# Kernel optimization log

Measured on AMD Instinct MI355X. Metric: run time of the kernel, lower is better.

The kernel has to match this reference:

```python
import jax, jax.numpy as jnp
import numpy as np

N_NODES = 50000
N_EDGES = 800000
N_GRAPHS = 64
NEG_SLOPE = 0.2  # PyG GATConv default negative_slope


def gat_conv(x, src, dst, W, att_src, att_dst, bias, heads, out_ch, concat):
    """PyG-style GATConv (eval mode, self-loops already in src/dst)."""
    N = x.shape[0]
    h = (x @ W).reshape(N, heads, out_ch)            # [N,H,C]
    a_s = jnp.sum(h * att_src, axis=-1)              # [N,H]
    a_d = jnp.sum(h * att_dst, axis=-1)              # [N,H]
    e = jax.nn.leaky_relu(a_s[src] + a_d[dst], NEG_SLOPE)  # [E,H]
    # segment softmax over incoming edges of each dst node
    m = jax.ops.segment_max(e, dst, num_segments=N)
    m = jnp.where(jnp.isfinite(m), m, 0.0)
    ex = jnp.exp(e - m[dst])
    denom = jax.ops.segment_sum(ex, dst, num_segments=N)
    alpha = ex / (denom[dst] + 1e-16)                # [E,H]
    out = jax.ops.segment_sum(alpha[:, :, None] * h[src], dst, num_segments=N)  # [N,H,C]
    out = out.reshape(N, heads * out_ch) if concat else out.mean(axis=1)
    return out + bias


def setup_inputs() -> dict:
    key = jax.random.key(0)
    ks = jax.random.split(key, 12)
    x = jax.random.normal(ks[0], (N_NODES, 5), dtype=jnp.float32)
    edge_index = jax.random.randint(ks[1], (2, N_EDGES), 0, N_NODES, dtype=jnp.int64)
    batch = jnp.sort(jax.random.randint(ks[2], (N_NODES,), 0, N_GRAPHS, dtype=jnp.int64))
    def glorot(k, shape):
        fan_in, fan_out = shape[0], shape[-1]
        s = jnp.sqrt(6.0 / (fan_in + fan_out))
        return jax.random.uniform(k, shape, jnp.float32, -s, s)
    return {
        "x": x,
        "edge_index": edge_index,
        "batch": batch,
        "W1": glorot(ks[3], (5, 256)),
        "att_src1": glorot(ks[4], (4, 64)),
        "att_dst1": glorot(ks[5], (4, 64)),
        "b1": jnp.zeros((256,), jnp.float32),
        "W2": glorot(ks[6], (256, 64)),
        "att_src2": glorot(ks[7], (1, 64)),
        "att_dst2": glorot(ks[8], (1, 64)),
        "b2": jnp.zeros((64,), jnp.float32),
        "lin_W": glorot(ks[9], (64, 2)),
        "lin_b": jnp.zeros((2,), jnp.float32),
    }


def reference(x, edge_index, batch, W1, att_src1, att_dst1, b1,
              W2, att_src2, att_dst2, b2, lin_W, lin_b):
    N = x.shape[0]
    loops = jnp.arange(N, dtype=edge_index.dtype)
    src = jnp.concatenate([edge_index[0], loops])
    dst = jnp.concatenate([edge_index[1], loops])
    h = jax.nn.relu(gat_conv(x, src, dst, W1, att_src1, att_dst1, b1, 4, 64, True))
    h = jax.nn.relu(gat_conv(h, src, dst, W2, att_src2, att_dst2, b2, 1, 64, False))
    # global mean pool over graphs
    sums = jax.ops.segment_sum(h, batch, num_segments=N_GRAPHS)          # [G,64]
    cnts = jax.ops.segment_sum(jnp.ones((N,), h.dtype), batch, num_segments=N_GRAPHS)
    pooled = sums / jnp.maximum(cnts, 1.0)[:, None]
    return pooled @ lin_W + lin_b
```

## Files before the change

### kernel.cpp

```cpp
#include <hip/hip_runtime.h>
#include <math.h>

#define N_NODES 50000
#define N_EDGES 800000
#define N_GRAPHS 64
#define NEG_SLOPE 0.2f
#define N_REP 64
#define ZERO_INT4 ((N_NODES * 4 + N_REP * N_GRAPHS * 64 * 4) / 16)
#define FILL_GRID 2048
#define NPX (N_NODES / 8)
#define SLOT 64

typedef __attribute__((ext_vector_type(8))) short short8;
typedef __attribute__((ext_vector_type(4))) float f32x4;

__device__ __forceinline__ float lrelu(float x) { return x > 0.f ? x : NEG_SLOPE * x; }

__device__ __forceinline__ unsigned short f2bf(float f) {
    union { float f; unsigned int u; } v; v.f = f;
    unsigned int r = (v.u + 0x7fffu + ((v.u >> 16) & 1u)) >> 16;
    return (unsigned short)r;
}
__device__ __forceinline__ float bf2f(unsigned short b) {
    union { unsigned int u; float f; } v; v.u = ((unsigned int)b) << 16;
    return v.f;
}
__device__ __forceinline__ float bfLO(unsigned int u) {
    union { unsigned int u; float f; } v; v.u = u << 16;
    return v.f;
}
__device__ __forceinline__ float bfHI(unsigned int u) {
    union { unsigned int u; float f; } v; v.u = u & 0xffff0000u;
    return v.f;
}

__device__ __forceinline__ int lower_bound_i(const int* __restrict__ a, int n, int v) {
    int lo = 0, hi = n;
    while (lo < hi) { int m = (lo + hi) >> 1; if (a[m] < v) lo = m + 1; else hi = m; }
    return lo;
}

__global__ __launch_bounds__(256) void k_gemm1(const float* __restrict__ x,
                                               const float* __restrict__ W1,
                                               const float* __restrict__ att_s,
                                               const float* __restrict__ att_d,
                                               float4* __restrict__ a_s,
                                               float4* __restrict__ a_d,
                                               int4* __restrict__ zp,
                                               float4* __restrict__ xp4) {
    __shared__ float Ws[5 * 256];
    const int t = threadIdx.x;
    {
        int tid = blockIdx.x * 256 + t;
        if (tid < ZERO_INT4) zp[tid] = make_int4(0, 0, 0, 0);
    }
    for (int i = t; i < 5 * 256; i += 256) Ws[i] = W1[i];
    __syncthreads();
    const int wave = t >> 6, lane = t & 63;
    const int n = blockIdx.x * 4 + wave;
    if (n >= N_NODES) return;
    float x0 = x[n * 5 + 0], x1 = x[n * 5 + 1], x2 = x[n * 5 + 2],
          x3 = x[n * 5 + 3], x4 = x[n * 5 + 4];
    if (lane == 0) {
        xp4[n * 2]     = make_float4(x0, x1, x2, x3);
        xp4[n * 2 + 1] = make_float4(x4, 0.f, 0.f, 0.f);
    }
    float vs[4], vd[4];
#pragma unroll
    for (int hd = 0; hd < 4; ++hd) {
        const int c = hd * 64 + lane;
        float h = x0 * Ws[c] + x1 * Ws[256 + c] + x2 * Ws[512 + c] +
                  x3 * Ws[768 + c] + x4 * Ws[1024 + c];
        vs[hd] = h * att_s[c];
        vd[hd] = h * att_d[c];
    }
#pragma unroll
    for (int off = 32; off; off >>= 1) {
#pragma unroll
        for (int hd = 0; hd < 4; ++hd) {
            vs[hd] += __shfl_xor(vs[hd], off, 64);
            vd[hd] += __shfl_xor(vd[hd], off, 64);
        }
    }
    if (lane == 0) {
        a_s[n] = make_float4(vs[0], vs[1], vs[2], vs[3]);
        a_d[n] = make_float4(vd[0], vd[1], vd[2], vd[3]);
    }
}

__global__ __launch_bounds__(256) void k_fill2(const int* __restrict__ src,
                                               const int* __restrict__ dst,
                                               int* __restrict__ cnt,
                                               int* __restrict__ csr_src) {
    const int r = blockIdx.x & 7;
    const int slice = blockIdx.x >> 3;
    const int lo = r * NPX;
    const int per = (N_EDGES + (FILL_GRID / 8) - 1) / (FILL_GRID / 8);
    const int e0 = slice * per;
    const int e1 = min(e0 + per, N_EDGES);
    for (int e = e0 + threadIdx.x; e < e1; e += 256) {
        int d = dst[e];
        if ((unsigned)(d - lo) < (unsigned)NPX) {
            int rk = atomicAdd(&cnt[d], 1);
            if (rk < SLOT) csr_src[(d << 6) + rk] = src[e];
        }
    }
}

__global__ __launch_bounds__(256) void k_agg1(const float4* __restrict__ xp4,
                                              const float* __restrict__ W1,
                                              const float4* __restrict__ asv,
                                              const float4* __restrict__ adv,
                                              const int* __restrict__ cnt,
                                              const int* __restrict__ csr_src,
                                              const float* __restrict__ b1,
                                              unsigned short* __restrict__ out1rm) {
    __shared__ float hand[4][4][24];
    const int t = threadIdx.x;
    const int wave = t >> 6, lane = t & 63;
    const int grp = lane >> 4, l16 = lane & 15;
    const int d = blockIdx.x * 16 + wave * 4 + grp;

    float w1r[4][5], bias[4];
#pragma unroll
    for (int h = 0; h < 4; ++h) {
#pragma unroll
        for (int i = 0; i < 5; ++i) w1r[h][i] = W1[i * 256 + h * 64 + lane];
        bias[h] = b1[h * 64 + lane];
    }

    const int beg = d << 6;
    const int end = beg + min(cnt[d], SLOT);
    const float4 ad = adv[d];

    float den[4] = {0.f, 0.f, 0.f, 0.f};
    float xw[4][5];
#pragma unroll
    for (int h = 0; h < 4; ++h)
#pragma unroll
        for (int i = 0; i < 5; ++i) xw[h][i] = 0.f;

    for (int cb = beg; cb < end; cb += 16) {
        const int j = cb + l16;
        if (j < end) {
            const int s = csr_src[j];
            const float4 a = asv[s];
            float w[4];
            w[0] = __expf(lrelu(a.x + ad.x));
            w[1] = __expf(lrelu(a.y + ad.y));
            w[2] = __expf(lrelu(a.z + ad.z));
            w[3] = __expf(lrelu(a.w + ad.w));
            float4 xa = xp4[2 * s];
            float4 xb = xp4[2 * s + 1];
            float xv[5] = {xa.x, xa.y, xa.z, xa.w, xb.x};
#pragma unroll
            for (int h = 0; h < 4; ++h) {
                den[h] += w[h];
#pragma unroll
                for (int i = 0; i < 5; ++i) xw[h][i] += w[h] * xv[i];
            }
        }
    }

#pragma unroll
    for (int off = 1; off < 16; off <<= 1) {
#pragma unroll
        for (int h = 0; h < 4; ++h) {
            den[h] += __shfl_xor(den[h], off, 64);
#pragma unroll
            for (int i = 0; i < 5; ++i) xw[h][i] += __shfl_xor(xw[h][i], off, 64);
        }
    }

    {
        const float4 as = asv[d];
        float w[4];
        w[0] = __expf(lrelu(as.x + ad.x));
        w[1] = __expf(lrelu(as.y + ad.y));
        w[2] = __expf(lrelu(as.z + ad.z));
        w[3] = __expf(lrelu(as.w + ad.w));
        float4 xa = xp4[2 * d];
        float4 xb = xp4[2 * d + 1];
        float xv[5] = {xa.x, xa.y, xa.z, xa.w, xb.x};
#pragma unroll
        for (int h = 0; h < 4; ++h) {
            den[h] += w[h];
#pragma unroll
            for (int i = 0; i < 5; ++i) xw[h][i] += w[h] * xv[i];
        }
    }

    if (l16 == 0) {
#pragma unroll
        for (int h = 0; h < 4; ++h) hand[wave][grp][h] = den[h];
#pragma unroll
        for (int h = 0; h < 4; ++h)
#pragma unroll
            for (int i = 0; i < 5; ++i) hand[wave][grp][4 + h * 5 + i] = xw[h][i];
    }
    __syncthreads();

#pragma unroll
    for (int n = 0; n < 4; ++n) {
        const int dn = blockIdx.x * 16 + wave * 4 + n;
        unsigned short* op = out1rm + (size_t)dn * 256;
#pragma unroll
        for (int h = 0; h < 4; ++h) {
            const float dh = hand[wave][n][h] + 1e-16f;
            float hh = hand[wave][n][4 + h * 5 + 0] * w1r[h][0]
                     + hand[wave][n][4 + h * 5 + 1] * w1r[h][1]
                     + hand[wave][n][4 + h * 5 + 2] * w1r[h][2]
                     + hand[wave][n][4 + h * 5 + 3] * w1r[h][3]
                     + hand[wave][n][4 + h * 5 + 4] * w1r[h][4];
            op[h * 64 + lane] = f2bf(fmaxf(hh / dh + bias[h], 0.f));
        }
    }
}

__global__ __launch_bounds__(256) void k_gemm2(const unsigned short* __restrict__ in,
                                               const float* __restrict__ W2,
                                               const float* __restrict__ att_s2,
                                               const float* __restrict__ att_d2,
                                               unsigned short* __restrict__ h2b,
                                               float* __restrict__ a_s2,
                                               float* __restrict__ a_d2) {
    __shared__ unsigned short lW[16384];
    const int t = threadIdx.x;
    for (int idx = t; idx < 16384; idx += 256) {
        int j = idx & 7, c16 = (idx >> 3) & 15, tt = (idx >> 7) & 3,
            g = (idx >> 9) & 3, s = idx >> 11;
        int k = 32 * s + 8 * g + j, c = 16 * tt + c16;
        lW[idx] = f2bf(W2[k * 64 + c]);
    }
    __syncthreads();
    const int wave = t >> 6, lane = t & 63;
    const int g = lane >> 4, c16 = lane & 15;
    const int nb = blockIdx.x * 64 + wave * 16;
    if (nb >= N_NODES) return;

    f32x4 acc[4];
#pragma unroll
    for (int i = 0; i < 4; ++i) acc[i] = (f32x4){0.f, 0.f, 0.f, 0.f};

    const unsigned short* arow = in + (size_t)(nb + c16) * 256;
#pragma unroll
    for (int s = 0; s < 8; ++s) {
        short8 a = *reinterpret_cast<const short8*>(arow + 32 * s + 8 * g);
#pragma unroll
        for (int tt = 0; tt < 4; ++tt) {
            short8 b = *reinterpret_cast<const short8*>(
                lW + ((((s * 4 + g) * 4 + tt) * 16 + c16) << 3));
            acc[tt] = __builtin_amdgcn_mfma_f32_16x16x32_bf16(a, b, acc[tt], 0, 0, 0);
        }
    }

    float attS[4], attD[4];
#pragma unroll
    for (int tt = 0; tt < 4; ++tt) {
        attS[tt] = att_s2[16 * tt + c16];
        attD[tt] = att_d2[16 * tt + c16];
    }
#pragma unroll
    for (int r = 0; r < 4; ++r) {
        const int node = nb + g * 4 + r;
        const bool ok = node < N_NODES;
        float vs = 0.f, vd = 0.f;
#pragma unroll
        for (int tt = 0; tt < 4; ++tt) {
            float v = acc[tt][r];
            if (ok) h2b[(size_t)node * 64 + 16 * tt + c16] = f2bf(v);
            vs += v * attS[tt];
            vd += v * attD[tt];
        }
#pragma unroll
        for (int off = 1; off < 16; off <<= 1) {
            vs += __shfl_xor(vs, off, 64);
            vd += __shfl_xor(vd, off, 64);
        }
        if (ok && c16 == 0) { a_s2[node] = vs; a_d2[node] = vd; }
    }
}

__global__ __launch_bounds__(256) void k_agg2(const unsigned int* __restrict__ h2u,
                                              const float* __restrict__ as_,
                                              const float* __restrict__ ad_,
                                              const int* __restrict__ cnt,
                                              const int* __restrict__ csr_src,
                                              const float* __restrict__ b2,
                                              const int* __restrict__ batch,
                                              float* __restrict__ sums) {
    __shared__ int2 ew[4][2][32];
    const int t = threadIdx.x;
    const int wid = t >> 6, lane = t & 63;
    const int g = lane >> 5, m = lane & 31;
    const int d = blockIdx.x * 8 + wid * 2 + g;
    const int beg = d << 6;
    const int end = beg + min(cnt[d], SLOT);
    const float adl = ad_[d];

    float den = 0.f, accx = 0.f, accy = 0.f;
    for (int c = beg; c < end; c += 32) {
        int rem = end - c; if (rem > 32) rem = 32;
        if (m < rem) {
            int s = csr_src[c + m];
            float w = __expf(lrelu(as_[s] + adl));
            den += w;
            ew[wid][g][m] = make_int2(s, __float_as_int(w));
        }
        int e = 0;
        for (; e + 4 <= rem; e += 4) {
            int2 p0 = ew[wid][g][e],     p1 = ew[wid][g][e + 1];
            int2 p2 = ew[wid][g][e + 2], p3 = ew[wid][g][e + 3];
            unsigned int v0 = h2u[(size_t)p0.x * 32 + m];
            unsigned int v1 = h2u[(size_t)p1.x * 32 + m];
            unsigned int v2 = h2u[(size_t)p2.x * 32 + m];
            unsigned int v3 = h2u[(size_t)p3.x * 32 + m];
            float w0 = __int_as_float(p0.y), w1 = __int_as_float(p1.y);
            float w2 = __int_as_float(p2.y), w3 = __int_as_float(p3.y);
            accx += w0 * bfLO(v0); accy += w0 * bfHI(v0);
            accx += w1 * bfLO(v1); accy += w1 * bfHI(v1);
            accx += w2 * bfLO(v2); accy += w2 * bfHI(v2);
            accx += w3 * bfLO(v3); accy += w3 * bfHI(v3);
        }
        for (; e < rem; ++e) {
            int2 p = ew[wid][g][e];
            unsigned int v = h2u[(size_t)p.x * 32 + m];
            float w = __int_as_float(p.y);
            accx += w * bfLO(v); accy += w * bfHI(v);
        }
    }
#pragma unroll
    for (int off = 16; off; off >>= 1) den += __shfl_xor(den, off, 64);
    {
        float w = __expf(lrelu(as_[d] + adl));
        den += w;
        unsigned int v = h2u[(size_t)d * 32 + m];
        accx += w * bfLO(v); accy += w * bfHI(v);
    }
    float inv = 1.0f / (den + 1e-16f);
    float v0 = fmaxf(accx * inv + b2[2 * m], 0.f);
    float v1 = fmaxf(accy * inv + b2[2 * m + 1], 0.f);
    const int rep = ((blockIdx.x << 3) + (wid << 1) + g) & (N_REP - 1);
    float* sb = sums + (size_t)rep * (N_GRAPHS * 64) + batch[d] * 64;
    atomicAdd(&sb[2 * m], v0);
    atomicAdd(&sb[2 * m + 1], v1);
}

__global__ __launch_bounds__(64) void k_final(const float* __restrict__ sums,
                                              const int* __restrict__ batch,
                                              const float* __restrict__ linW,
                                              const float* __restrict__ linb,
                                              float* __restrict__ out) {
    const int g = blockIdx.x;
    const int lane = threadIdx.x;
    float s = 0.f;
#pragma unroll 8
    for (int r = 0; r < N_REP; ++r)
        s += sums[(size_t)r * (N_GRAPHS * 64) + g * 64 + lane];
    int beg = lower_bound_i(batch, N_NODES, g);
    int end = lower_bound_i(batch, N_NODES, g + 1);
    float val = s / fmaxf((float)(end - beg), 1.0f);
    float v0 = val * linW[lane * 2 + 0];
    float v1 = val * linW[lane * 2 + 1];
#pragma unroll
    for (int off = 32; off; off >>= 1) {
        v0 += __shfl_xor(v0, off, 64);
        v1 += __shfl_xor(v1, off, 64);
    }
    if (lane == 0) {
        out[g * 2 + 0] = v0 + linb[0];
        out[g * 2 + 1] = v1 + linb[1];
    }
}

extern "C" void kernel_launch(void* const* d_in, const int* in_sizes, int n_in,
                              void* d_out, int out_size, void* d_ws, size_t ws_size,
                              hipStream_t stream) {
    const float* x    = (const float*)d_in[0];
    const int*   ei   = (const int*)d_in[1];
    const int*   bat  = (const int*)d_in[2];
    const float* W1   = (const float*)d_in[3];
    const float* as1  = (const float*)d_in[4];
    const float* ad1  = (const float*)d_in[5];
    const float* b1   = (const float*)d_in[6];
    const float* W2   = (const float*)d_in[7];
    const float* as2  = (const float*)d_in[8];
    const float* ad2  = (const float*)d_in[9];
    const float* b2   = (const float*)d_in[10];
    const float* linW = (const float*)d_in[11];
    const float* linb = (const float*)d_in[12];
    float* out = (float*)d_out;

    const int* src = ei;
    const int* dst = ei + N_EDGES;

    char* w = (char*)d_ws;
    unsigned short* out1rm = (unsigned short*)w; w += (size_t)N_NODES * 256 * 2;
    float4* a_s1 = (float4*)w; w += (size_t)N_NODES * 16;
    float4* a_d1 = (float4*)w; w += (size_t)N_NODES * 16;
    unsigned short* h2b = (unsigned short*)w; w += (size_t)N_NODES * 64 * 2;
    float* a_s2  = (float*)w; w += (size_t)N_NODES * 4;
    float* a_d2  = (float*)w; w += (size_t)N_NODES * 4;
    int* counts  = (int*)w;   w += (size_t)N_NODES * 4;
    float* sums  = (float*)w; w += (size_t)N_REP * N_GRAPHS * 64 * 4;
    int* csr_src = (int*)w;   w += (size_t)N_NODES * SLOT * 4;
    float4* xp4  = (float4*)w; w += (size_t)N_NODES * 32;

    k_gemm1<<<(N_NODES + 3) / 4, 256, 0, stream>>>(x, W1, as1, ad1, a_s1, a_d1,
                                                   (int4*)counts, xp4);
    k_fill2<<<FILL_GRID, 256, 0, stream>>>(src, dst, counts, csr_src);

    k_agg1<<<N_NODES / 16, 256, 0, stream>>>(xp4, W1, a_s1, a_d1, counts, csr_src, b1, out1rm);
    k_gemm2<<<(N_NODES + 63) / 64, 256, 0, stream>>>(out1rm, W2, as2, ad2, h2b, a_s2, a_d2);
    k_agg2<<<N_NODES / 8, 256, 0, stream>>>((const unsigned int*)h2b, a_s2, a_d2,
                                            counts, csr_src, b2, bat, sums);
    k_final<<<N_GRAPHS, 64, 0, stream>>>(sums, bat, linW, linb, out);
}
```

Baseline: 182.7 us.

## Fuse layer-1 aggregation with layer-2 GEMM via shared-memory staging

The layer-1 aggregation kernel now keeps its 16 output rows in LDS as bf16 and runs the layer-2 MFMA GEMM plus attention-score reduction in the same block, so the 25.6MB out1 intermediate is never written to or read back from global memory and one launch goes away. The W2 bf16 pre-swizzle moves into k_gemm1, writing to a global buffer that each fused block reads directly instead of rebuilding a 32KB LDS copy per block. In exchange, each wave does one MFMA tile, the kernel uses more LDS and adds barriers, and B operands are read from global/L2 rather than LDS.

```diff
diff --git a/kernel.cpp b/kernel.cpp
--- a/kernel.cpp
+++ b/kernel.cpp
@@ -10,6 +10,7 @@
 #define FILL_GRID 2048
 #define NPX (N_NODES / 8)
 #define SLOT 64
+#define O1LD 264
 
 typedef __attribute__((ext_vector_type(8))) short short8;
 typedef __attribute__((ext_vector_type(4))) float f32x4;
@@ -44,15 +45,24 @@
                                                const float* __restrict__ W1,
                                                const float* __restrict__ att_s,
                                                const float* __restrict__ att_d,
+                                               const float* __restrict__ W2,
                                                float4* __restrict__ a_s,
                                                float4* __restrict__ a_d,
                                                int4* __restrict__ zp,
-                                               float4* __restrict__ xp4) {
+                                               float4* __restrict__ xp4,
+                                               unsigned short* __restrict__ lWg) {
     __shared__ float Ws[5 * 256];
     const int t = threadIdx.x;
     {
         int tid = blockIdx.x * 256 + t;
         if (tid < ZERO_INT4) zp[tid] = make_int4(0, 0, 0, 0);
+    }
+    if (blockIdx.x < 64) {
+        int idx = blockIdx.x * 256 + t;
+        int j = idx & 7, c16 = (idx >> 3) & 15, tt = (idx >> 7) & 3,
+            g = (idx >> 9) & 3, s = idx >> 11;
+        int k = 32 * s + 8 * g + j, c = 16 * tt + c16;
+        lWg[idx] = f2bf(W2[k * 64 + c]);
     }
     for (int i = t; i < 5 * 256; i += 256) Ws[i] = W1[i];
     __syncthreads();
@@ -107,19 +117,27 @@
     }
 }
 
-__global__ __launch_bounds__(256) void k_agg1(const float4* __restrict__ xp4,
+__global__ __launch_bounds__(256) void k_fuse(const float4* __restrict__ xp4,
                                               const float* __restrict__ W1,
                                               const float4* __restrict__ asv,
                                               const float4* __restrict__ adv,
                                               const int* __restrict__ cnt,
                                               const int* __restrict__ csr_src,
                                               const float* __restrict__ b1,
-                                              unsigned short* __restrict__ out1rm) {
+                                              const unsigned short* __restrict__ lWg,
+                                              const float* __restrict__ att_s2,
+                                              const float* __restrict__ att_d2,
+                                              unsigned short* __restrict__ h2b,
+                                              float* __restrict__ a_s2,
+                                              float* __restrict__ a_d2) {
+    __shared__ unsigned short o1[16][O1LD];
     __shared__ float hand[4][4][24];
+    __shared__ float vsp[4][16][2];
     const int t = threadIdx.x;
     const int wave = t >> 6, lane = t & 63;
     const int grp = lane >> 4, l16 = lane & 15;
-    const int d = blockIdx.x * 16 + wave * 4 + grp;
+    const int nb = blockIdx.x * 16;
+    const int d = nb + wave * 4 + grp;
 
     float w1r[4][5], bias[4];
 #pragma unroll
@@ -202,8 +220,7 @@
 
 #pragma unroll
     for (int n = 0; n < 4; ++n) {
-        const int dn = blockIdx.x * 16 + wave * 4 + n;
-        unsigned short* op = out1rm + (size_t)dn * 256;
+        const int nl = wave * 4 + n;
 #pragma unroll
         for (int h = 0; h < 4; ++h) {
             const float dh = hand[wave][n][h] + 1e-16f;
@@ -212,72 +229,46 @@
                      + hand[wave][n][4 + h * 5 + 2] * w1r[h][2]
                      + hand[wave][n][4 + h * 5 + 3] * w1r[h][3]
                      + hand[wave][n][4 + h * 5 + 4] * w1r[h][4];
-            op[h * 64 + lane] = f2bf(fmaxf(hh / dh + bias[h], 0.f));
-        }
-    }
-}
-
-__global__ __launch_bounds__(256) void k_gemm2(const unsigned short* __restrict__ in,
-                                               const float* __restrict__ W2,
-                                               const float* __restrict__ att_s2,
-                                               const float* __restrict__ att_d2,
-                                               unsigned short* __restrict__ h2b,
-                                               float* __restrict__ a_s2,
-                                               float* __restrict__ a_d2) {
-    __shared__ unsigned short lW[16384];
-    const int t = threadIdx.x;
-    for (int idx = t; idx < 16384; idx += 256) {
-        int j = idx & 7, c16 = (idx >> 3) & 15, tt = (idx >> 7) & 3,
-            g = (idx >> 9) & 3, s = idx >> 11;
-        int k = 32 * s + 8 * g + j, c = 16 * tt + c16;
-        lW[idx] = f2bf(W2[k * 64 + c]);
+            o1[nl][h * 64 + lane] = f2bf(fmaxf(hh / dh + bias[h], 0.f));
+        }
     }
     __syncthreads();
-    const int wave = t >> 6, lane = t & 63;
+
+    const int tt = wave;
     const int g = lane >> 4, c16 = lane & 15;
-    const int nb = blockIdx.x * 64 + wave * 16;
-    if (nb >= N_NODES) return;
-
-    f32x4 acc[4];
-#pragma unroll
-    for (int i = 0; i < 4; ++i) acc[i] = (f32x4){0.f, 0.f, 0.f, 0.f};
-
-    const unsigned short* arow = in + (size_t)(nb + c16) * 256;
+    f32x4 acc = (f32x4){0.f, 0.f, 0.f, 0.f};
 #pragma unroll
     for (int s = 0; s < 8; ++s) {
-        short8 a = *reinterpret_cast<const short8*>(arow + 32 * s + 8 * g);
-#pragma unroll
-        for (int tt = 0; tt < 4; ++tt) {
-            short8 b = *reinterpret_cast<const short8*>(
-                lW + ((((s * 4 + g) * 4 + tt) * 16 + c16) << 3));
-            acc[tt] = __builtin_amdgcn_mfma_f32_16x16x32_bf16(a, b, acc[tt], 0, 0, 0);
-        }
-    }
-
-    float attS[4], attD[4];
-#pragma unroll
-    for (int tt = 0; tt < 4; ++tt) {
-        attS[tt] = att_s2[16 * tt + c16];
-        attD[tt] = att_d2[16 * tt + c16];
-    }
+        short8 a = *reinterpret_cast<const short8*>(&o1[c16][32 * s + 8 * g]);
+        short8 b = *reinterpret_cast<const short8*>(
+            lWg + ((((s * 4 + g) * 4 + tt) * 16 + c16) << 3));
+        acc = __builtin_amdgcn_mfma_f32_16x16x32_bf16(a, b, acc, 0, 0, 0);
+    }
+
+    const float attS = att_s2[16 * tt + c16];
+    const float attD = att_d2[16 * tt + c16];
 #pragma unroll
     for (int r = 0; r < 4; ++r) {
         const int node = nb + g * 4 + r;
-        const bool ok = node < N_NODES;
-        float vs = 0.f, vd = 0.f;
-#pragma unroll
-        for (int tt = 0; tt < 4; ++tt) {
-            float v = acc[tt][r];
-            if (ok) h2b[(size_t)node * 64 + 16 * tt + c16] = f2bf(v);
-            vs += v * attS[tt];
-            vd += v * attD[tt];
-        }
+        float v = acc[r];
+        h2b[(size_t)node * 64 + 16 * tt + c16] = f2bf(v);
+        float vs = v * attS, vd = v * attD;
 #pragma unroll
         for (int off = 1; off < 16; off <<= 1) {
             vs += __shfl_xor(vs, off, 64);
             vd += __shfl_xor(vd, off, 64);
         }
-        if (ok && c16 == 0) { a_s2[node] = vs; a_d2[node] = vd; }
+        if (c16 == 0) {
+            vsp[tt][g * 4 + r][0] = vs;
+            vsp[tt][g * 4 + r][1] = vd;
+        }
+    }
+    __syncthreads();
+    if (t < 16) {
+        float vs = vsp[0][t][0] + vsp[1][t][0] + vsp[2][t][0] + vsp[3][t][0];
+        float vd = vsp[0][t][1] + vsp[1][t][1] + vsp[2][t][1] + vsp[3][t][1];
+        a_s2[nb + t] = vs;
+        a_d2[nb + t] = vd;
     }
 }
 
@@ -395,7 +386,6 @@
     const int* dst = ei + N_EDGES;
 
     char* w = (char*)d_ws;
-    unsigned short* out1rm = (unsigned short*)w; w += (size_t)N_NODES * 256 * 2;
     float4* a_s1 = (float4*)w; w += (size_t)N_NODES * 16;
     float4* a_d1 = (float4*)w; w += (size_t)N_NODES * 16;
     unsigned short* h2b = (unsigned short*)w; w += (size_t)N_NODES * 64 * 2;
@@ -405,13 +395,14 @@
     float* sums  = (float*)w; w += (size_t)N_REP * N_GRAPHS * 64 * 4;
     int* csr_src = (int*)w;   w += (size_t)N_NODES * SLOT * 4;
     float4* xp4  = (float4*)w; w += (size_t)N_NODES * 32;
-
-    k_gemm1<<<(N_NODES + 3) / 4, 256, 0, stream>>>(x, W1, as1, ad1, a_s1, a_d1,
-                                                   (int4*)counts, xp4);
+    unsigned short* lWg = (unsigned short*)w; w += 16384 * 2;
+
+    k_gemm1<<<(N_NODES + 3) / 4, 256, 0, stream>>>(x, W1, as1, ad1, W2, a_s1, a_d1,
+                                                   (int4*)counts, xp4, lWg);
     k_fill2<<<FILL_GRID, 256, 0, stream>>>(src, dst, counts, csr_src);
 
-    k_agg1<<<N_NODES / 16, 256, 0, stream>>>(xp4, W1, a_s1, a_d1, counts, csr_src, b1, out1rm);
-    k_gemm2<<<(N_NODES + 63) / 64, 256, 0, stream>>>(out1rm, W2, as2, ad2, h2b, a_s2, a_d2);
+    k_fuse<<<N_NODES / 16, 256, 0, stream>>>(xp4, W1, a_s1, a_d1, counts, csr_src,
+                                             b1, lWg, as2, ad2, h2b, a_s2, a_d2);
     k_agg2<<<N_NODES / 8, 256, 0, stream>>>((const unsigned int*)h2b, a_s2, a_d2,
                                             counts, csr_src, b2, bat, sums);
     k_final<<<N_GRAPHS, 64, 0, stream>>>(sums, bat, linW, linb, out);
```

New measurement: 179.2 us. No clear change (-1.9%).
